# Kernel optimization log

Measured on AMD Instinct MI355X. Metric: run time of the kernel, lower is better.

Reference implementation:

```python
import jax, jax.numpy as jnp
import numpy as np

N_NODES = 100000
N_EDGES = 600000
D_IN = 128
D_OUT = 128


def setup_inputs() -> dict:
    key = jax.random.key(0)
    k1, k2, k3, k4, k5, k6 = jax.random.split(key, 6)
    node_feature = jax.random.normal(k1, (N_NODES, D_IN), dtype=jnp.float32)
    edge_indices = jax.random.randint(k2, (2, N_EDGES), 0, N_NODES, dtype=jnp.int64)
    scale = 1.0 / np.sqrt(D_IN)
    W_line = jax.random.uniform(k3, (D_OUT, D_IN), jnp.float32, -scale, scale)
    b_line = jax.random.uniform(k4, (D_OUT,), jnp.float32, -scale, scale)
    W_self = jax.random.uniform(k5, (D_OUT, D_IN), jnp.float32, -scale, scale)
    b_self = jax.random.uniform(k6, (D_OUT,), jnp.float32, -scale, scale)
    return {
        "node_feature": node_feature,
        "edge_indices": edge_indices,
        "W_line": W_line,
        "b_line": b_line,
        "W_self": W_self,
        "b_self": b_self,
    }


def reference(node_feature, edge_indices, W_line, b_line, W_self, b_self):
    source = edge_indices[0]
    target = edge_indices[1]
    # gather source features along edges: [E, D_in]
    src_feat = node_feature[source]
    # scatter-mean into target nodes (torch_scatter mean: sum / max(count,1))
    seg_sum = jax.ops.segment_sum(src_feat, target, num_segments=N_NODES)
    count = jax.ops.segment_sum(
        jnp.ones((src_feat.shape[0],), dtype=node_feature.dtype),
        target, num_segments=N_NODES)
    mean = seg_sum / jnp.maximum(count, 1.0)[:, None]
    # neighbour linear + self linear
    out = (mean @ W_line.T + b_line) + (node_feature @ W_self.T + b_self)
    return out
```

## Files before the change

### kernel.cpp

```cpp
#include <hip/hip_runtime.h>

#define N_NODES 100000
#define N_EDGES 600000
#define D 128
#define M_PAD 100096

#define NB   196
#define BWID 512
#define NCH  196
#define CE   3062
#define SCAN_N (NB * NCH)
#define SCAN_BLK 151

typedef unsigned int uint32;
typedef unsigned long long uint64;
typedef __attribute__((ext_vector_type(8))) short short8;
typedef __attribute__((ext_vector_type(4))) float f32x4;

__device__ __forceinline__ uint32 f2bf(float x) {
    uint32 u = __float_as_uint(x);
    return (u + 0x7FFFu + ((u >> 16) & 1u)) >> 16;
}
__device__ __forceinline__ float bflo(uint32 u) { return __uint_as_float(u << 16); }
__device__ __forceinline__ float bfhi(uint32 u) { return __uint_as_float(u & 0xFFFF0000u); }

__global__ __launch_bounds__(256) void k1_convert_count(
        const float* __restrict__ nf, unsigned short* __restrict__ Abuf,
        const int* __restrict__ edges, uint32* __restrict__ cntmat,
        uint64* __restrict__ flags) {
    __shared__ uint32 c[NB];
    const int tid = threadIdx.x;
    const int bid = blockIdx.x;

    if (bid == 1023 && tid < SCAN_BLK) flags[tid] = 0ULL;

    for (int idx = bid * 256 + tid; idx < N_NODES * 16; idx += 1024 * 256) {
        int r = idx >> 4;
        int ccol = (idx & 15) * 8;
        const float4 v0 = *reinterpret_cast<const float4*>(nf + (size_t)r * D + ccol);
        const float4 v1 = *reinterpret_cast<const float4*>(nf + (size_t)r * D + ccol + 4);
        uint4 w;
        w.x = f2bf(v0.x) | (f2bf(v0.y) << 16);
        w.y = f2bf(v0.z) | (f2bf(v0.w) << 16);
        w.z = f2bf(v1.x) | (f2bf(v1.y) << 16);
        w.w = f2bf(v1.z) | (f2bf(v1.w) << 16);
        *reinterpret_cast<uint4*>(Abuf + (size_t)r * 256 + D + ccol) = w;
    }

    if (bid < NCH) {
        for (int i = tid; i < NB; i += 256) c[i] = 0u;
        __syncthreads();
        const int e0 = bid * CE;
        const int e1 = (e0 + CE < N_EDGES) ? e0 + CE : N_EDGES;
        for (int e = e0 + tid; e < e1; e += 256) {
            int tgt = edges[N_EDGES + e];
            atomicAdd(&c[tgt >> 9], 1u);
        }
        __syncthreads();
        for (int i = tid; i < NB; i += 256)
            cntmat[(size_t)i * NCH + bid] = c[i];
    }
}

__global__ __launch_bounds__(256) void k2_scan(
        uint32* __restrict__ cntmat, uint64* __restrict__ flags,
        const float* __restrict__ Wl, const float* __restrict__ Ws,
        const float* __restrict__ bl, const float* __restrict__ bs,
        unsigned short* __restrict__ WcF, float* __restrict__ biasc) {
    const int gidx = blockIdx.x * 256 + threadIdx.x;
    if (gidx < 4096) {
        int lane = gidx & 63, f2 = gidx >> 6;
        int ks = f2 & 7, nn = (f2 >> 3) & 3, ch = f2 >> 5;
        int j = ch * 64 + nn * 16 + (lane & 15);
        int kb = ks * 32 + (lane >> 4) * 8;
        const float* srcp = (kb < D) ? (Wl + (size_t)j * D + kb)
                                     : (Ws + (size_t)j * D + (kb - D));
        const float4 v0 = *reinterpret_cast<const float4*>(srcp);
        const float4 v1 = *reinterpret_cast<const float4*>(srcp + 4);
        uint4 w;
        w.x = f2bf(v0.x) | (f2bf(v0.y) << 16);
        w.y = f2bf(v0.z) | (f2bf(v0.w) << 16);
        w.z = f2bf(v1.x) | (f2bf(v1.y) << 16);
        w.w = f2bf(v1.z) | (f2bf(v1.w) << 16);
        *reinterpret_cast<uint4*>(WcF + (size_t)gidx * 8) = w;
    }
    if (gidx < D) biasc[gidx] = bl[gidx] + bs[gidx];

    __shared__ uint32 s[256];
    __shared__ uint32 r2[256];
    const int t = threadIdx.x;
    const int b = blockIdx.x;
    const int i = b * 256 + t;
    const uint32 v = (i < SCAN_N) ? cntmat[i] : 0u;
    s[t] = v;
    __syncthreads();
    for (int d = 1; d < 256; d <<= 1) {
        uint32 add = (t >= d) ? s[t - d] : 0u;
        __syncthreads();
        s[t] += add;
        __syncthreads();
    }
    const uint32 incl = s[t];
    const uint32 total = s[255];
    if (t == 0) atomicExch(&flags[b], (1ULL << 32) | (uint64)total);
    uint32 agg = 0;
    if (t < b) {
        uint64 fv;
        do { fv = atomicAdd(&flags[t], 0ULL); } while ((fv >> 32) == 0ULL);
        agg = (uint32)fv;
    }
    r2[t] = agg;
    __syncthreads();
    for (int d2 = 128; d2 > 0; d2 >>= 1) {
        if (t < d2) r2[t] += r2[t + d2];
        __syncthreads();
    }
    if (i < SCAN_N) cntmat[i] = r2[0] + incl - v;
}

__global__ __launch_bounds__(256) void k3_bucket(
        const int* __restrict__ edges, const uint32* __restrict__ base,
        uint32* __restrict__ bpair) {
    __shared__ uint32 c[NB];
    __shared__ uint32 bb[NB];
    const int t = threadIdx.x;
    const int cid = blockIdx.x;
    for (int i = t; i < NB; i += 256) {
        c[i] = 0u;
        bb[i] = base[(size_t)i * NCH + cid];
    }
    __syncthreads();
    const int e0 = cid * CE;
    const int e1 = (e0 + CE < N_EDGES) ? e0 + CE : N_EDGES;
    for (int e = e0 + t; e < e1; e += 256) {
        uint32 src = (uint32)edges[e];
        uint32 tgt = (uint32)edges[N_EDGES + e];
        uint32 bkt = tgt >> 9;
        uint32 r = atomicAdd(&c[bkt], 1u);
        uint32 pos = bb[bkt] + r;
        *reinterpret_cast<uint2*>(&bpair[2 * (size_t)pos]) = make_uint2(src, tgt);
    }
}

__global__ __launch_bounds__(256) void k4_csr(
        const uint32* __restrict__ bpair, const uint32* __restrict__ base,
        uint32* __restrict__ off, uint32* __restrict__ sorted_src) {
    __shared__ uint32 h[BWID];
    __shared__ uint32 h2[BWID];
    __shared__ uint32 pr[256];
    const int t = threadIdx.x;
    const int b = blockIdx.x;
    const uint32 start = base[(size_t)b * NCH];
    const uint32 end = (b == NB - 1) ? N_EDGES : base[(size_t)(b + 1) * NCH];
    for (int i = t; i < BWID; i += 256) { h[i] = 0u; h2[i] = 0u; }
    __syncthreads();
    for (uint32 e = start + t; e < end; e += 256) {
        uint32 tgt = bpair[2 * (size_t)e + 1];
        atomicAdd(&h[tgt & (BWID - 1)], 1u);
    }
    __syncthreads();
    const uint32 e0c = h[2 * t];
    const uint32 e1c = h[2 * t + 1];
    pr[t] = e0c + e1c;
    __syncthreads();
    for (int d = 1; d < 256; d <<= 1) {
        uint32 add = (t >= d) ? pr[t - d] : 0u;
        __syncthreads();
        pr[t] += add;
        __syncthreads();
    }
    const uint32 exb = (t > 0) ? pr[t - 1] : 0u;
    const int node0 = b * BWID + 2 * t;
    if (node0 < N_NODES) off[node0] = start + exb;
    if (node0 + 1 < N_NODES) off[node0 + 1] = start + exb + e0c;
    if (b == NB - 1 && t == 0) off[N_NODES] = N_EDGES;
    h[2 * t] = exb;
    h[2 * t + 1] = exb + e0c;
    __syncthreads();
    for (uint32 e = start + t; e < end; e += 256) {
        uint2 pq = *reinterpret_cast<const uint2*>(&bpair[2 * (size_t)e]);
        uint32 lt = pq.y & (BWID - 1);
        uint32 r = atomicAdd(&h2[lt], 1u);
        sorted_src[start + h[lt] + r] = pq.x;
    }
}

__global__ __launch_bounds__(256) void k_gather(
        const unsigned short* __restrict__ AbufC,
        unsigned short* __restrict__ Abuf,
        const uint32* __restrict__ off,
        const uint32* __restrict__ sorted_src) {
    const int wave = threadIdx.x >> 6;
    const int lane = threadIdx.x & 63;
    const int sub  = (lane >> 4) & 1;
    const int cl   = lane & 15;
    const int node = blockIdx.x * 8 + wave * 2 + (lane >> 5);
    const uint32 o = off[node];
    const uint32 d = off[node + 1] - o;
    const uint32* __restrict__ src = sorted_src + o;

#define LD(s) (*reinterpret_cast<const uint4*>(AbufC + (size_t)(s) * 256 + D + cl * 8))
#define ACC(a, u) { a[0] += bflo(u.x); a[1] += bfhi(u.x); a[2] += bflo(u.y); a[3] += bfhi(u.y); \
                    a[4] += bflo(u.z); a[5] += bfhi(u.z); a[6] += bflo(u.w); a[7] += bfhi(u.w); }

    float aA[8] = {0.f,0.f,0.f,0.f,0.f,0.f,0.f,0.f};
    float aB[8] = {0.f,0.f,0.f,0.f,0.f,0.f,0.f,0.f};
    uint32 j = 0;
    for (; j + 8 <= d; j += 8) {
        uint32 s0 = src[j + 0 + sub];
        uint32 s1 = src[j + 2 + sub];
        uint32 s2 = src[j + 4 + sub];
        uint32 s3 = src[j + 6 + sub];
        uint4 u0 = LD(s0); uint4 u1 = LD(s1); uint4 u2 = LD(s2); uint4 u3 = LD(s3);
        ACC(aA, u0); ACC(aA, u1); ACC(aB, u2); ACC(aB, u3);
    }
    if (j < d) {
        const uint32 dm1 = d - 1;
        uint32 i0 = j + 0 + sub, i1 = j + 2 + sub, i2 = j + 4 + sub, i3 = j + 6 + sub;
        uint32 s0 = src[i0 < dm1 ? i0 : dm1];
        uint32 s1 = src[i1 < dm1 ? i1 : dm1];
        uint32 s2 = src[i2 < dm1 ? i2 : dm1];
        uint32 s3 = src[i3 < dm1 ? i3 : dm1];
        uint4 u0 = LD(s0); uint4 u1 = LD(s1); uint4 u2 = LD(s2); uint4 u3 = LD(s3);
        if (i0 >= d) { u0.x = 0u; u0.y = 0u; u0.z = 0u; u0.w = 0u; }
        if (i1 >= d) { u1.x = 0u; u1.y = 0u; u1.z = 0u; u1.w = 0u; }
        if (i2 >= d) { u2.x = 0u; u2.y = 0u; u2.z = 0u; u2.w = 0u; }
        if (i3 >= d) { u3.x = 0u; u3.y = 0u; u3.z = 0u; u3.w = 0u; }
        ACC(aA, u0); ACC(aA, u1); ACC(aB, u2); ACC(aB, u3);
    }
#undef LD
#undef ACC
#pragma unroll
    for (int r = 0; r < 8; ++r) {
        aA[r] += aB[r];
        aA[r] += __shfl_xor(aA[r], 16);
    }
    if (sub == 0) {
        const float inv = 1.0f / (float)(d > 0u ? d : 1u);
        uint4 w;
        w.x = f2bf(aA[0] * inv) | (f2bf(aA[1] * inv) << 16);
        w.y = f2bf(aA[2] * inv) | (f2bf(aA[3] * inv) << 16);
        w.z = f2bf(aA[4] * inv) | (f2bf(aA[5] * inv) << 16);
        w.w = f2bf(aA[6] * inv) | (f2bf(aA[7] * inv) << 16);
        *reinterpret_cast<uint4*>(Abuf + (size_t)node * 256 + cl * 8) = w;
    }
}

__global__ __launch_bounds__(256) void sage_mfma(
        const unsigned short* __restrict__ Abuf,
        const unsigned short* __restrict__ WcF,
        const float* __restrict__ biasc,
        float* __restrict__ out) {
    __shared__ unsigned short WcL[16384];
    const int tid = threadIdx.x;
    const int rb = blockIdx.x >> 1;
    const int ch = blockIdx.x & 1;

    const unsigned short* wsrc = WcF + (size_t)ch * 16384;
#pragma unroll
    for (int i = 0; i < 8; ++i) {
        const int o = (i * 256 + tid) * 8;
        *reinterpret_cast<short8*>(&WcL[o]) = *reinterpret_cast<const short8*>(wsrc + o);
    }
    __syncthreads();

    const int wave = tid >> 6;
    const int lane = tid & 63;
    const int lr = lane & 15;
    const int lk = (lane >> 4) * 8;
    const long long row0 = (long long)rb * 64 + wave * 16;

    f32x4 acc[4];
#pragma unroll
    for (int n = 0; n < 4; ++n) acc[n] = (f32x4){0.f, 0.f, 0.f, 0.f};

    const unsigned short* pa = Abuf + (row0 + lr) * 256 + lk;
#pragma unroll
    for (int ks = 0; ks < 8; ++ks) {
        short8 a = *reinterpret_cast<const short8*>(pa + ks * 32);
#pragma unroll
        for (int n = 0; n < 4; ++n) {
            short8 b = *reinterpret_cast<const short8*>(&WcL[((n * 8 + ks) * 64 + lane) * 8]);
            acc[n] = __builtin_amdgcn_mfma_f32_16x16x32_bf16(a, b, acc[n], 0, 0, 0);
        }
    }

    float bv[4];
#pragma unroll
    for (int n = 0; n < 4; ++n) bv[n] = biasc[ch * 64 + n * 16 + lr];

    const int rq = (lane >> 4) * 4;
#pragma unroll
    for (int r = 0; r < 4; ++r) {
        const long long row = row0 + rq + r;
        if (row < N_NODES) {
            float* orow = out + row * D + ch * 64;
#pragma unroll
            for (int n = 0; n < 4; ++n)
                orow[n * 16 + lr] = acc[n][r] + bv[n];
        }
    }
}

extern "C" void kernel_launch(void* const* d_in, const int* in_sizes, int n_in,
                              void* d_out, int out_size, void* d_ws, size_t ws_size,
                              hipStream_t stream) {
    const float* nf    = (const float*)d_in[0];
    const int*   edges = (const int*)d_in[1];
    const float* Wl    = (const float*)d_in[2];
    const float* bl    = (const float*)d_in[3];
    const float* Ws    = (const float*)d_in[4];
    const float* bs    = (const float*)d_in[5];
    float* out = (float*)d_out;

    char* p = (char*)d_ws;
    unsigned short* Abuf = (unsigned short*)p; p += (size_t)M_PAD * 256 * sizeof(unsigned short);
    uint32* cntmat     = (uint32*)p; p += (size_t)40000 * sizeof(uint32);
    uint32* bpair      = (uint32*)p; p += (size_t)2 * N_EDGES * sizeof(uint32);
    uint32* sorted_src = (uint32*)p; p += (size_t)N_EDGES * sizeof(uint32);
    uint32* off        = (uint32*)p; p += (size_t)(N_NODES + 8) * sizeof(uint32);
    uint64* flags      = (uint64*)p; p += 2048;
    unsigned short* WcF = (unsigned short*)p; p += (size_t)D * 256 * sizeof(unsigned short);
    float* biasc       = (float*)p;

    k1_convert_count<<<1024, 256, 0, stream>>>(nf, Abuf, edges, cntmat, flags);
    k2_scan<<<SCAN_BLK, 256, 0, stream>>>(cntmat, flags, Wl, Ws, bl, bs, WcF, biasc);
    k3_bucket<<<NCH, 256, 0, stream>>>(edges, cntmat, bpair);
    k4_csr<<<NB, 256, 0, stream>>>(bpair, cntmat, off, sorted_src);
    k_gather<<<N_NODES / 8, 256, 0, stream>>>(Abuf, Abuf, off, sorted_src);
    sage_mfma<<<(M_PAD / 64) * 2, 256, 0, stream>>>(Abuf, WcF, biasc, out);
}
```

Measured before the change: 97.67 us.

## Fuse scan and bucket kernels with flag-based sync, pack edge pairs, unroll gather

Merges the decoupled-lookback scan and the bucketing pass into one kernel. Each block scans one bucket row, publishes its offsets with a ready flag in a 64-bit count matrix, then spins on the flags of its column before scattering edges. Edge pairs are packed into a single 32-bit word (local target index in the high bits, source in the low 17), which halves bpair traffic in the bucket and CSR kernels. The gather loop is unrolled to 16 neighbours per iteration to keep more loads in flight. The trade-off is that the kernel relies on all 196 blocks being co-resident to avoid spin deadlock, and the gather now uses more registers.

Result: slower. 100.8 us (+3.2%).

```diff
diff --git a/kernel.cpp b/kernel.cpp
--- a/kernel.cpp
+++ b/kernel.cpp
@@ -9,8 +9,6 @@
 #define BWID 512
 #define NCH  196
 #define CE   3062
-#define SCAN_N (NB * NCH)
-#define SCAN_BLK 151
 
 typedef unsigned int uint32;
 typedef unsigned long long uint64;
@@ -26,13 +24,13 @@
 
 __global__ __launch_bounds__(256) void k1_convert_count(
         const float* __restrict__ nf, unsigned short* __restrict__ Abuf,
-        const int* __restrict__ edges, uint32* __restrict__ cntmat,
+        const int* __restrict__ edges, uint64* __restrict__ cntmat,
         uint64* __restrict__ flags) {
     __shared__ uint32 c[NB];
     const int tid = threadIdx.x;
     const int bid = blockIdx.x;
 
-    if (bid == 1023 && tid < SCAN_BLK) flags[tid] = 0ULL;
+    if (bid == 1023 && tid < NB) flags[tid] = 0ULL;
 
     for (int idx = bid * 256 + tid; idx < N_NODES * 16; idx += 1024 * 256) {
         int r = idx >> 4;
@@ -58,16 +56,20 @@
         }
         __syncthreads();
         for (int i = tid; i < NB; i += 256)
-            cntmat[(size_t)i * NCH + bid] = c[i];
-    }
-}
-
-__global__ __launch_bounds__(256) void k2_scan(
-        uint32* __restrict__ cntmat, uint64* __restrict__ flags,
+            cntmat[(size_t)i * NCH + bid] = (uint64)c[i];
+    }
+}
+
+__global__ __launch_bounds__(256) void k23_scan_bucket(
+        const int* __restrict__ edges, uint64* __restrict__ cntmat,
+        uint64* __restrict__ flags,
         const float* __restrict__ Wl, const float* __restrict__ Ws,
         const float* __restrict__ bl, const float* __restrict__ bs,
-        unsigned short* __restrict__ WcF, float* __restrict__ biasc) {
-    const int gidx = blockIdx.x * 256 + threadIdx.x;
+        unsigned short* __restrict__ WcF, float* __restrict__ biasc,
+        uint32* __restrict__ bpair) {
+    const int t = threadIdx.x;
+    const int b = blockIdx.x;
+    const int gidx = b * 256 + t;
     if (gidx < 4096) {
         int lane = gidx & 63, f2 = gidx >> 6;
         int ks = f2 & 7, nn = (f2 >> 3) & 3, ch = f2 >> 5;
@@ -88,10 +90,11 @@
 
     __shared__ uint32 s[256];
     __shared__ uint32 r2[256];
-    const int t = threadIdx.x;
-    const int b = blockIdx.x;
-    const int i = b * 256 + t;
-    const uint32 v = (i < SCAN_N) ? cntmat[i] : 0u;
+    __shared__ uint32 c[NB];
+    __shared__ uint32 bb[NB];
+
+    uint32 v = 0;
+    if (t < NCH) v = (uint32)cntmat[(size_t)b * NCH + t];
     s[t] = v;
     __syncthreads();
     for (int d = 1; d < 256; d <<= 1) {
@@ -115,48 +118,43 @@
         if (t < d2) r2[t] += r2[t + d2];
         __syncthreads();
     }
-    if (i < SCAN_N) cntmat[i] = r2[0] + incl - v;
-}
-
-__global__ __launch_bounds__(256) void k3_bucket(
-        const int* __restrict__ edges, const uint32* __restrict__ base,
-        uint32* __restrict__ bpair) {
-    __shared__ uint32 c[NB];
-    __shared__ uint32 bb[NB];
-    const int t = threadIdx.x;
-    const int cid = blockIdx.x;
-    for (int i = t; i < NB; i += 256) {
-        c[i] = 0u;
-        bb[i] = base[(size_t)i * NCH + cid];
-    }
-    __syncthreads();
-    const int e0 = cid * CE;
+    const uint32 blockbase = r2[0];
+    if (t < NCH)
+        atomicExch(&cntmat[(size_t)b * NCH + t],
+                   (1ULL << 32) | (uint64)(blockbase + incl - v));
+
+    if (t < NB) {
+        uint64 e;
+        do { e = atomicAdd(&cntmat[(size_t)t * NCH + b], 0ULL); } while ((e >> 32) == 0ULL);
+        bb[t] = (uint32)e;
+        c[t] = 0u;
+    }
+    __syncthreads();
+    const int e0 = b * CE;
     const int e1 = (e0 + CE < N_EDGES) ? e0 + CE : N_EDGES;
     for (int e = e0 + t; e < e1; e += 256) {
         uint32 src = (uint32)edges[e];
         uint32 tgt = (uint32)edges[N_EDGES + e];
         uint32 bkt = tgt >> 9;
         uint32 r = atomicAdd(&c[bkt], 1u);
-        uint32 pos = bb[bkt] + r;
-        *reinterpret_cast<uint2*>(&bpair[2 * (size_t)pos]) = make_uint2(src, tgt);
+        bpair[bb[bkt] + r] = ((tgt & 511u) << 17) | src;
     }
 }
 
 __global__ __launch_bounds__(256) void k4_csr(
-        const uint32* __restrict__ bpair, const uint32* __restrict__ base,
+        const uint32* __restrict__ bpair, const uint64* __restrict__ base,
         uint32* __restrict__ off, uint32* __restrict__ sorted_src) {
     __shared__ uint32 h[BWID];
     __shared__ uint32 h2[BWID];
     __shared__ uint32 pr[256];
     const int t = threadIdx.x;
     const int b = blockIdx.x;
-    const uint32 start = base[(size_t)b * NCH];
-    const uint32 end = (b == NB - 1) ? N_EDGES : base[(size_t)(b + 1) * NCH];
+    const uint32 start = (uint32)base[(size_t)b * NCH];
+    const uint32 end = (b == NB - 1) ? N_EDGES : (uint32)base[(size_t)(b + 1) * NCH];
     for (int i = t; i < BWID; i += 256) { h[i] = 0u; h2[i] = 0u; }
     __syncthreads();
     for (uint32 e = start + t; e < end; e += 256) {
-        uint32 tgt = bpair[2 * (size_t)e + 1];
-        atomicAdd(&h[tgt & (BWID - 1)], 1u);
+        atomicAdd(&h[bpair[e] >> 17], 1u);
     }
     __syncthreads();
     const uint32 e0c = h[2 * t];
@@ -178,10 +176,10 @@
     h[2 * t + 1] = exb + e0c;
     __syncthreads();
     for (uint32 e = start + t; e < end; e += 256) {
-        uint2 pq = *reinterpret_cast<const uint2*>(&bpair[2 * (size_t)e]);
-        uint32 lt = pq.y & (BWID - 1);
+        uint32 pq = bpair[e];
+        uint32 lt = pq >> 17;
         uint32 r = atomicAdd(&h2[lt], 1u);
-        sorted_src[start + h[lt] + r] = pq.x;
+        sorted_src[start + h[lt] + r] = pq & 0x1FFFFu;
     }
 }
 
@@ -206,27 +204,44 @@
     float aA[8] = {0.f,0.f,0.f,0.f,0.f,0.f,0.f,0.f};
     float aB[8] = {0.f,0.f,0.f,0.f,0.f,0.f,0.f,0.f};
     uint32 j = 0;
-    for (; j + 8 <= d; j += 8) {
-        uint32 s0 = src[j + 0 + sub];
-        uint32 s1 = src[j + 2 + sub];
-        uint32 s2 = src[j + 4 + sub];
-        uint32 s3 = src[j + 6 + sub];
+    for (; j + 16 <= d; j += 16) {
+        uint32 s0 = src[j +  0 + sub];
+        uint32 s1 = src[j +  2 + sub];
+        uint32 s2 = src[j +  4 + sub];
+        uint32 s3 = src[j +  6 + sub];
+        uint32 s4 = src[j +  8 + sub];
+        uint32 s5 = src[j + 10 + sub];
+        uint32 s6 = src[j + 12 + sub];
+        uint32 s7 = src[j + 14 + sub];
         uint4 u0 = LD(s0); uint4 u1 = LD(s1); uint4 u2 = LD(s2); uint4 u3 = LD(s3);
+        uint4 u4 = LD(s4); uint4 u5 = LD(s5); uint4 u6 = LD(s6); uint4 u7 = LD(s7);
         ACC(aA, u0); ACC(aA, u1); ACC(aB, u2); ACC(aB, u3);
+        ACC(aA, u4); ACC(aA, u5); ACC(aB, u6); ACC(aB, u7);
     }
     if (j < d) {
         const uint32 dm1 = d - 1;
-        uint32 i0 = j + 0 + sub, i1 = j + 2 + sub, i2 = j + 4 + sub, i3 = j + 6 + sub;
+        uint32 i0 = j +  0 + sub, i1 = j +  2 + sub, i2 = j +  4 + sub, i3 = j +  6 + sub;
+        uint32 i4 = j +  8 + sub, i5 = j + 10 + sub, i6 = j + 12 + sub, i7 = j + 14 + sub;
         uint32 s0 = src[i0 < dm1 ? i0 : dm1];
         uint32 s1 = src[i1 < dm1 ? i1 : dm1];
         uint32 s2 = src[i2 < dm1 ? i2 : dm1];
         uint32 s3 = src[i3 < dm1 ? i3 : dm1];
+        uint32 s4 = src[i4 < dm1 ? i4 : dm1];
+        uint32 s5 = src[i5 < dm1 ? i5 : dm1];
+        uint32 s6 = src[i6 < dm1 ? i6 : dm1];
+        uint32 s7 = src[i7 < dm1 ? i7 : dm1];
         uint4 u0 = LD(s0); uint4 u1 = LD(s1); uint4 u2 = LD(s2); uint4 u3 = LD(s3);
+        uint4 u4 = LD(s4); uint4 u5 = LD(s5); uint4 u6 = LD(s6); uint4 u7 = LD(s7);
         if (i0 >= d) { u0.x = 0u; u0.y = 0u; u0.z = 0u; u0.w = 0u; }
         if (i1 >= d) { u1.x = 0u; u1.y = 0u; u1.z = 0u; u1.w = 0u; }
         if (i2 >= d) { u2.x = 0u; u2.y = 0u; u2.z = 0u; u2.w = 0u; }
         if (i3 >= d) { u3.x = 0u; u3.y = 0u; u3.z = 0u; u3.w = 0u; }
+        if (i4 >= d) { u4.x = 0u; u4.y = 0u; u4.z = 0u; u4.w = 0u; }
+        if (i5 >= d) { u5.x = 0u; u5.y = 0u; u5.z = 0u; u5.w = 0u; }
+        if (i6 >= d) { u6.x = 0u; u6.y = 0u; u6.z = 0u; u6.w = 0u; }
+        if (i7 >= d) { u7.x = 0u; u7.y = 0u; u7.z = 0u; u7.w = 0u; }
         ACC(aA, u0); ACC(aA, u1); ACC(aB, u2); ACC(aB, u3);
+        ACC(aA, u4); ACC(aA, u5); ACC(aB, u6); ACC(aB, u7);
     }
 #undef LD
 #undef ACC
@@ -315,8 +330,8 @@
 
     char* p = (char*)d_ws;
     unsigned short* Abuf = (unsigned short*)p; p += (size_t)M_PAD * 256 * sizeof(unsigned short);
-    uint32* cntmat     = (uint32*)p; p += (size_t)40000 * sizeof(uint32);
-    uint32* bpair      = (uint32*)p; p += (size_t)2 * N_EDGES * sizeof(uint32);
+    uint64* cntmat     = (uint64*)p; p += (size_t)(NB * NCH + 16) * sizeof(uint64);
+    uint32* bpair      = (uint32*)p; p += (size_t)N_EDGES * sizeof(uint32);
     uint32* sorted_src = (uint32*)p; p += (size_t)N_EDGES * sizeof(uint32);
     uint32* off        = (uint32*)p; p += (size_t)(N_NODES + 8) * sizeof(uint32);
     uint64* flags      = (uint64*)p; p += 2048;
@@ -324,8 +339,8 @@
     float* biasc       = (float*)p;
 
     k1_convert_count<<<1024, 256, 0, stream>>>(nf, Abuf, edges, cntmat, flags);
-    k2_scan<<<SCAN_BLK, 256, 0, stream>>>(cntmat, flags, Wl, Ws, bl, bs, WcF, biasc);
-    k3_bucket<<<NCH, 256, 0, stream>>>(edges, cntmat, bpair);
+    k23_scan_bucket<<<NB, 256, 0, stream>>>(edges, cntmat, flags, Wl, Ws, bl, bs,
+                                            WcF, biasc, bpair);
     k4_csr<<<NB, 256, 0, stream>>>(bpair, cntmat, off, sorted_src);
     k_gather<<<N_NODES / 8, 256, 0, stream>>>(Abuf, Abuf, off, sorted_src);
     sage_mfma<<<(M_PAD / 64) * 2, 256, 0, stream>>>(Abuf, WcF, biasc, out);
```

## Fuse neighbour-mean gather into MFMA GEMM via swizzled LDS tile

Applied to the files above, without the earlier changes.

Merges the gather/mean kernel and the MFMA linear kernel into one 512-thread kernel. Each block aggregates the mean features of its 64 nodes into a swizzled shared-memory tile, then runs the GEMM, taking the mean half from LDS and the self half from a compact bf16 node buffer. This removes the global write and re-read of the aggregated features and one launch, and halves the bf16 buffer row stride. In exchange each block loads the full 64KB combined weight into LDS and needs about 80KB of shared memory, which lowers occupancy. The gather phase may also stall the MFMA phase within a block.

Measured after the change: 95.64 us. 1.02x faster.

```diff
diff --git a/kernel.cpp b/kernel.cpp
--- a/kernel.cpp
+++ b/kernel.cpp
@@ -25,7 +25,7 @@
 __device__ __forceinline__ float bfhi(uint32 u) { return __uint_as_float(u & 0xFFFF0000u); }
 
 __global__ __launch_bounds__(256) void k1_convert_count(
-        const float* __restrict__ nf, unsigned short* __restrict__ Abuf,
+        const float* __restrict__ nf, unsigned short* __restrict__ AbufN,
         const int* __restrict__ edges, uint32* __restrict__ cntmat,
         uint64* __restrict__ flags) {
     __shared__ uint32 c[NB];
@@ -44,7 +44,7 @@
         w.y = f2bf(v0.z) | (f2bf(v0.w) << 16);
         w.z = f2bf(v1.x) | (f2bf(v1.y) << 16);
         w.w = f2bf(v1.z) | (f2bf(v1.w) << 16);
-        *reinterpret_cast<uint4*>(Abuf + (size_t)r * 256 + D + ccol) = w;
+        *reinterpret_cast<uint4*>(AbufN + (size_t)r * 128 + ccol) = w;
     }
 
     if (bid < NCH) {
@@ -185,116 +185,132 @@
     }
 }
 
-__global__ __launch_bounds__(256) void k_gather(
-        const unsigned short* __restrict__ AbufC,
-        unsigned short* __restrict__ Abuf,
+__global__ __launch_bounds__(512) void k_fused(
+        const unsigned short* __restrict__ AbufN,
         const uint32* __restrict__ off,
-        const uint32* __restrict__ sorted_src) {
-    const int wave = threadIdx.x >> 6;
-    const int lane = threadIdx.x & 63;
-    const int sub  = (lane >> 4) & 1;
-    const int cl   = lane & 15;
-    const int node = blockIdx.x * 8 + wave * 2 + (lane >> 5);
-    const uint32 o = off[node];
-    const uint32 d = off[node + 1] - o;
-    const uint32* __restrict__ src = sorted_src + o;
-
-#define LD(s) (*reinterpret_cast<const uint4*>(AbufC + (size_t)(s) * 256 + D + cl * 8))
-#define ACC(a, u) { a[0] += bflo(u.x); a[1] += bfhi(u.x); a[2] += bflo(u.y); a[3] += bfhi(u.y); \
-                    a[4] += bflo(u.z); a[5] += bfhi(u.z); a[6] += bflo(u.w); a[7] += bfhi(u.w); }
-
-    float aA[8] = {0.f,0.f,0.f,0.f,0.f,0.f,0.f,0.f};
-    float aB[8] = {0.f,0.f,0.f,0.f,0.f,0.f,0.f,0.f};
-    uint32 j = 0;
-    for (; j + 8 <= d; j += 8) {
-        uint32 s0 = src[j + 0 + sub];
-        uint32 s1 = src[j + 2 + sub];
-        uint32 s2 = src[j + 4 + sub];
-        uint32 s3 = src[j + 6 + sub];
-        uint4 u0 = LD(s0); uint4 u1 = LD(s1); uint4 u2 = LD(s2); uint4 u3 = LD(s3);
-        ACC(aA, u0); ACC(aA, u1); ACC(aB, u2); ACC(aB, u3);
-    }
-    if (j < d) {
-        const uint32 dm1 = d - 1;
-        uint32 i0 = j + 0 + sub, i1 = j + 2 + sub, i2 = j + 4 + sub, i3 = j + 6 + sub;
-        uint32 s0 = src[i0 < dm1 ? i0 : dm1];
-        uint32 s1 = src[i1 < dm1 ? i1 : dm1];
-        uint32 s2 = src[i2 < dm1 ? i2 : dm1];
-        uint32 s3 = src[i3 < dm1 ? i3 : dm1];
-        uint4 u0 = LD(s0); uint4 u1 = LD(s1); uint4 u2 = LD(s2); uint4 u3 = LD(s3);
-        if (i0 >= d) { u0.x = 0u; u0.y = 0u; u0.z = 0u; u0.w = 0u; }
-        if (i1 >= d) { u1.x = 0u; u1.y = 0u; u1.z = 0u; u1.w = 0u; }
-        if (i2 >= d) { u2.x = 0u; u2.y = 0u; u2.z = 0u; u2.w = 0u; }
-        if (i3 >= d) { u3.x = 0u; u3.y = 0u; u3.z = 0u; u3.w = 0u; }
-        ACC(aA, u0); ACC(aA, u1); ACC(aB, u2); ACC(aB, u3);
-    }
-#undef LD
-#undef ACC
-#pragma unroll
-    for (int r = 0; r < 8; ++r) {
-        aA[r] += aB[r];
-        aA[r] += __shfl_xor(aA[r], 16);
-    }
-    if (sub == 0) {
-        const float inv = 1.0f / (float)(d > 0u ? d : 1u);
-        uint4 w;
-        w.x = f2bf(aA[0] * inv) | (f2bf(aA[1] * inv) << 16);
-        w.y = f2bf(aA[2] * inv) | (f2bf(aA[3] * inv) << 16);
-        w.z = f2bf(aA[4] * inv) | (f2bf(aA[5] * inv) << 16);
-        w.w = f2bf(aA[6] * inv) | (f2bf(aA[7] * inv) << 16);
-        *reinterpret_cast<uint4*>(Abuf + (size_t)node * 256 + cl * 8) = w;
-    }
-}
-
-__global__ __launch_bounds__(256) void sage_mfma(
-        const unsigned short* __restrict__ Abuf,
+        const uint32* __restrict__ sorted_src,
         const unsigned short* __restrict__ WcF,
         const float* __restrict__ biasc,
         float* __restrict__ out) {
-    __shared__ unsigned short WcL[16384];
+    __shared__ unsigned short WcL[32768];
+    __shared__ unsigned short Am[8192];
     const int tid = threadIdx.x;
-    const int rb = blockIdx.x >> 1;
-    const int ch = blockIdx.x & 1;
-
-    const unsigned short* wsrc = WcF + (size_t)ch * 16384;
-#pragma unroll
-    for (int i = 0; i < 8; ++i) {
-        const int o = (i * 256 + tid) * 8;
-        *reinterpret_cast<short8*>(&WcL[o]) = *reinterpret_cast<const short8*>(wsrc + o);
-    }
-    __syncthreads();
-
     const int wave = tid >> 6;
     const int lane = tid & 63;
-    const int lr = lane & 15;
-    const int lk = (lane >> 4) * 8;
-    const long long row0 = (long long)rb * 64 + wave * 16;
+    const int row0 = blockIdx.x * 64;
+
+#pragma unroll
+    for (int i = 0; i < 8; ++i) {
+        const int o = (i * 512 + tid) * 8;
+        *reinterpret_cast<short8*>(&WcL[o]) = *reinterpret_cast<const short8*>(WcF + o);
+    }
+
+    const int sub = (lane >> 4) & 1;
+    const int cl  = lane & 15;
+    const int g   = lane >> 5;
+
+#define LD(s) (*reinterpret_cast<const uint4*>(AbufN + (size_t)(s) * 128 + cl * 8))
+#define ACC(a, u) { a[0] += bflo(u.x); a[1] += bfhi(u.x); a[2] += bflo(u.y); a[3] += bfhi(u.y); \
+                    a[4] += bflo(u.z); a[5] += bfhi(u.z); a[6] += bflo(u.w); a[7] += bfhi(u.w); }
+
+    for (int pr = 0; pr < 4; ++pr) {
+        const int nl = wave * 8 + pr * 2 + g;
+        const int node = row0 + nl;
+        float aA[8] = {0.f,0.f,0.f,0.f,0.f,0.f,0.f,0.f};
+        float aB[8] = {0.f,0.f,0.f,0.f,0.f,0.f,0.f,0.f};
+        uint32 d = 0;
+        if (node < N_NODES) {
+            const uint32 o = off[node];
+            d = off[node + 1] - o;
+            const uint32* __restrict__ src = sorted_src + o;
+            uint32 j = 0;
+            for (; j + 8 <= d; j += 8) {
+                uint32 s0 = src[j + 0 + sub];
+                uint32 s1 = src[j + 2 + sub];
+                uint32 s2 = src[j + 4 + sub];
+                uint32 s3 = src[j + 6 + sub];
+                uint4 u0 = LD(s0); uint4 u1 = LD(s1); uint4 u2 = LD(s2); uint4 u3 = LD(s3);
+                ACC(aA, u0); ACC(aA, u1); ACC(aB, u2); ACC(aB, u3);
+            }
+            if (j < d) {
+                const uint32 dm1 = d - 1;
+                uint32 i0 = j + 0 + sub, i1 = j + 2 + sub, i2 = j + 4 + sub, i3 = j + 6 + sub;
+                uint32 s0 = src[i0 < dm1 ? i0 : dm1];
+                uint32 s1 = src[i1 < dm1 ? i1 : dm1];
+                uint32 s2 = src[i2 < dm1 ? i2 : dm1];
+                uint32 s3 = src[i3 < dm1 ? i3 : dm1];
+                uint4 u0 = LD(s0); uint4 u1 = LD(s1); uint4 u2 = LD(s2); uint4 u3 = LD(s3);
+                if (i0 >= d) { u0.x = 0u; u0.y = 0u; u0.z = 0u; u0.w = 0u; }
+                if (i1 >= d) { u1.x = 0u; u1.y = 0u; u1.z = 0u; u1.w = 0u; }
+                if (i2 >= d) { u2.x = 0u; u2.y = 0u; u2.z = 0u; u2.w = 0u; }
+                if (i3 >= d) { u3.x = 0u; u3.y = 0u; u3.z = 0u; u3.w = 0u; }
+                ACC(aA, u0); ACC(aA, u1); ACC(aB, u2); ACC(aB, u3);
+            }
+        }
+#pragma unroll
+        for (int r = 0; r < 8; ++r) {
+            aA[r] += aB[r];
+            aA[r] += __shfl_xor(aA[r], 16);
+        }
+        if (sub == 0) {
+            const float inv = 1.0f / (float)(d > 0u ? d : 1u);
+            uint4 w;
+            w.x = f2bf(aA[0] * inv) | (f2bf(aA[1] * inv) << 16);
+            w.y = f2bf(aA[2] * inv) | (f2bf(aA[3] * inv) << 16);
+            w.z = f2bf(aA[4] * inv) | (f2bf(aA[5] * inv) << 16);
+            w.w = f2bf(aA[6] * inv) | (f2bf(aA[7] * inv) << 16);
+            *reinterpret_cast<uint4*>(&Am[nl * 128 + ((cl ^ (nl & 7)) * 8)]) = w;
+        }
+    }
+#undef LD
+#undef ACC
+    __syncthreads();
+
+    const int rg  = wave >> 1;
+    const int chh = wave & 1;
+    const int lr  = lane & 15;
+    const int lkq = lane >> 4;
+    const int lk  = lkq * 8;
+    const int arow = rg * 16 + lr;
 
     f32x4 acc[4];
 #pragma unroll
     for (int n = 0; n < 4; ++n) acc[n] = (f32x4){0.f, 0.f, 0.f, 0.f};
 
-    const unsigned short* pa = Abuf + (row0 + lr) * 256 + lk;
-#pragma unroll
-    for (int ks = 0; ks < 8; ++ks) {
-        short8 a = *reinterpret_cast<const short8*>(pa + ks * 32);
+#pragma unroll
+    for (int ks = 0; ks < 4; ++ks) {
+        const int c0 = lkq + ks * 4;
+        short8 a = *reinterpret_cast<const short8*>(
+            &Am[arow * 128 + ((c0 ^ (arow & 7)) * 8)]);
 #pragma unroll
         for (int n = 0; n < 4; ++n) {
-            short8 b = *reinterpret_cast<const short8*>(&WcL[((n * 8 + ks) * 64 + lane) * 8]);
+            short8 b = *reinterpret_cast<const short8*>(
+                &WcL[((chh * 32 + n * 8 + ks) * 64 + lane) * 8]);
             acc[n] = __builtin_amdgcn_mfma_f32_16x16x32_bf16(a, b, acc[n], 0, 0, 0);
         }
     }
+    const unsigned short* pa = AbufN + (size_t)(row0 + arow) * 128 + lk;
+#pragma unroll
+    for (int ks = 4; ks < 8; ++ks) {
+        short8 a = *reinterpret_cast<const short8*>(pa + (ks - 4) * 32);
+#pragma unroll
+        for (int n = 0; n < 4; ++n) {
+            short8 b = *reinterpret_cast<const short8*>(
+                &WcL[((chh * 32 + n * 8 + ks) * 64 + lane) * 8]);
+            acc[n] = __builtin_amdgcn_mfma_f32_16x16x32_bf16(a, b, acc[n], 0, 0, 0);
+        }
+    }
 
     float bv[4];
 #pragma unroll
-    for (int n = 0; n < 4; ++n) bv[n] = biasc[ch * 64 + n * 16 + lr];
-
-    const int rq = (lane >> 4) * 4;
+    for (int n = 0; n < 4; ++n) bv[n] = biasc[chh * 64 + n * 16 + lr];
+
+    const int rq = lkq * 4;
 #pragma unroll
     for (int r = 0; r < 4; ++r) {
-        const long long row = row0 + rq + r;
+        const int row = row0 + rg * 16 + rq + r;
         if (row < N_NODES) {
-            float* orow = out + row * D + ch * 64;
+            float* orow = out + (size_t)row * D + chh * 64;
 #pragma unroll
             for (int n = 0; n < 4; ++n)
                 orow[n * 16 + lr] = acc[n][r] + bv[n];
@@ -314,8 +330,8 @@
     float* out = (float*)d_out;
 
     char* p = (char*)d_ws;
-    unsigned short* Abuf = (unsigned short*)p; p += (size_t)M_PAD * 256 * sizeof(unsigned short);
-    uint32* cntmat     = (uint32*)p; p += (size_t)40000 * sizeof(uint32);
+    unsigned short* AbufN = (unsigned short*)p; p += (size_t)M_PAD * 128 * sizeof(unsigned short);
+    uint32* cntmat     = (uint32*)p; p += (size_t)(SCAN_N + 64) * sizeof(uint32);
     uint32* bpair      = (uint32*)p; p += (size_t)2 * N_EDGES * sizeof(uint32);
     uint32* sorted_src = (uint32*)p; p += (size_t)N_EDGES * sizeof(uint32);
     uint32* off        = (uint32*)p; p += (size_t)(N_NODES + 8) * sizeof(uint32);
@@ -323,10 +339,9 @@
     unsigned short* WcF = (unsigned short*)p; p += (size_t)D * 256 * sizeof(unsigned short);
     float* biasc       = (float*)p;
 
-    k1_convert_count<<<1024, 256, 0, stream>>>(nf, Abuf, edges, cntmat, flags);
+    k1_convert_count<<<1024, 256, 0, stream>>>(nf, AbufN, edges, cntmat, flags);
     k2_scan<<<SCAN_BLK, 256, 0, stream>>>(cntmat, flags, Wl, Ws, bl, bs, WcF, biasc);
     k3_bucket<<<NCH, 256, 0, stream>>>(edges, cntmat, bpair);
     k4_csr<<<NB, 256, 0, stream>>>(bpair, cntmat, off, sorted_src);
-    k_gather<<<N_NODES / 8, 256, 0, stream>>>(Abuf, Abuf, off, sorted_src);
-    sage_mfma<<<(M_PAD / 64) * 2, 256, 0, stream>>>(Abuf, WcF, biasc, out);
-}
+    k_fused<<<(N_NODES + 63) / 64, 512, 0, stream>>>(AbufN, off, sorted_src, WcF, biasc, out);
+}
```
